# Optimization experiments

Measured on AMD Instinct MI355X. Metric: run time of the kernel, lower is better.

## Reference

```python
import jax, jax.numpy as jnp
import numpy as np
from jax import lax

COND_RATE = 4  # para_cond_downscale_rate
DG = 8        # deformable_groups


def _conv(x, w, b, pad=0, groups=1):
    out = lax.conv_general_dilated(x, w, (1, 1), [(pad, pad), (pad, pad)],
                                   feature_group_count=groups,
                                   dimension_numbers=('NCHW', 'OIHW', 'NCHW'))
    return out + b[None, :, None, None]


def _gn(x, g, b, groups=32, eps=1e-6):
    B, C, H, W = x.shape
    xr = x.reshape(B, groups, C // groups, H * W)
    m = xr.mean(axis=(2, 3), keepdims=True)
    v = ((xr - m) ** 2).mean(axis=(2, 3), keepdims=True)
    xr = (xr - m) * lax.rsqrt(v + eps)
    return xr.reshape(B, C, H, W) * g[None, :, None, None] + b[None, :, None, None]


def _deform_conv2d(x, offset, mask, w, b, dg):
    # x: [B,Cin,H,W], offset: [B,2*dg*9,H,W] (torchvision layout: interleaved y,x per loc),
    # mask: [B,dg*9,H,W], w: [Cout,Cin,3,3]. stride=1, pad=1, dil=1, zero border.
    B, Cin, H, W = x.shape
    K = 9
    Cpg = Cin // dg
    Cout = w.shape[0]
    off = offset.reshape(B, dg, K, 2, H, W)
    ky = (jnp.arange(K) // 3).astype(x.dtype)
    kx = (jnp.arange(K) % 3).astype(x.dtype)
    iy = jnp.arange(H, dtype=x.dtype)
    ix = jnp.arange(W, dtype=x.dtype)
    base_y = iy[None, :, None] - 1.0 + ky[:, None, None]  # [K,H,1]
    base_x = ix[None, None, :] - 1.0 + kx[:, None, None]  # [K,1,W]
    py = off[:, :, :, 0] + base_y[None, None]  # [B,dg,K,H,W]
    px = off[:, :, :, 1] + base_x[None, None]
    y0 = jnp.floor(py)
    x0 = jnp.floor(px)
    ly = py - y0
    lx = px - x0
    xg = x.reshape(B, dg, Cpg, H * W)

    def corner(yc, xc, wt):
        valid = (yc >= 0) & (yc < H) & (xc >= 0) & (xc < W)
        yci = jnp.clip(yc, 0, H - 1).astype(jnp.int32)
        xci = jnp.clip(xc, 0, W - 1).astype(jnp.int32)
        idx = (yci * W + xci).reshape(B, dg, 1, K * H * W)
        v = jnp.take_along_axis(xg, idx, axis=3).reshape(B, dg, Cpg, K, H, W)
        return v * (wt * valid.astype(x.dtype))[:, :, None]

    samp = (corner(y0, x0, (1 - ly) * (1 - lx)) + corner(y0, x0 + 1, (1 - ly) * lx)
            + corner(y0 + 1, x0, ly * (1 - lx)) + corner(y0 + 1, x0 + 1, ly * lx))
    samp = samp * mask.reshape(B, dg, 1, K, H, W)
    wr = w.reshape(Cout, dg, Cpg, K)
    out = jnp.einsum('bgckhw,ogck->bohw', samp, wr)
    return out + b[None, :, None, None]


def setup_inputs() -> dict:
    key = jax.random.key(0)
    ks = jax.random.split(key, 10)
    C = 256
    f32 = jnp.float32
    d = {}
    d['main_feature'] = jax.random.normal(ks[0], (8, C, 64, 64), f32)
    d['condition_feature'] = jax.random.normal(ks[1], (8, C, 16, 16), f32)
    # offset_conv1: 1x1 -> GN -> SiLU -> depthwise 7x7 -> GN -> SiLU -> 1x1
    d['w1'] = jax.random.normal(ks[2], (C, 2 * C, 1, 1), f32) * 0.03
    d['b1'] = jnp.zeros((C,), f32)
    d['g1'] = jnp.ones((C,), f32)
    d['be1'] = jnp.zeros((C,), f32)
    d['w2'] = jax.random.normal(ks[3], (C, 1, 7, 7), f32) * 0.05
    d['b2'] = jnp.zeros((C,), f32)
    d['g2'] = jnp.ones((C,), f32)
    d['be2'] = jnp.zeros((C,), f32)
    d['w3'] = jax.random.normal(ks[4], (C, C, 1, 1), f32) * 0.03
    d['b3'] = jnp.zeros((C,), f32)
    # offset_conv2: 3x3 -> GN -> SiLU
    d['w4'] = jax.random.normal(ks[5], (C, C, 3, 3), f32) * 0.02
    d['b4'] = jnp.zeros((C,), f32)
    d['g3'] = jnp.ones((C,), f32)
    d['be3'] = jnp.zeros((C,), f32)
    # DCNv2Pack conv_offset: 3x3 -> 3*dg*9 = 216 channels (small init -> small offsets)
    d['w_co'] = jax.random.normal(ks[6], (3 * DG * 9, C, 3, 3), f32) * 0.01
    d['b_co'] = jnp.zeros((3 * DG * 9,), f32)
    # DCN main weight
    d['w_dcn'] = jax.random.normal(ks[7], (C, C, 3, 3), f32) * 0.02
    d['b_dcn'] = jnp.zeros((C,), f32)
    return d


def reference(main_feature, condition_feature, w1, b1, g1, be1, w2, b2, g2, be2,
              w3, b3, w4, b4, g3, be3, w_co, b_co, w_dcn, b_dcn):
    B, Cc, h, w_ = condition_feature.shape
    _, Cm, H, W = main_feature.shape
    # note: 2 // cond_downscale_rate == 0 for rate=4, so first resize is identity-sized
    cond = jax.image.resize(condition_feature, (B, Cc, h + 2 // COND_RATE, w_ + 2 // COND_RATE), 'bilinear')
    cond = jax.image.resize(cond, (B, Cc, H, W), 'bilinear')
    f = jnp.concatenate([cond, main_feature], axis=1)
    f = _conv(f, w1, b1)
    f = jax.nn.silu(_gn(f, g1, be1))
    f = _conv(f, w2, b2, pad=3, groups=Cm)  # depthwise 7x7
    f = jax.nn.silu(_gn(f, g2, be2))
    f = _conv(f, w3, b3)
    f = _conv(f, w4, b4, pad=1)
    offset_feat = jax.nn.silu(_gn(f, g3, be3))
    co = _conv(offset_feat, w_co, b_co, pad=1)  # [B, 3*dg*9, H, W]
    o1, o2, m = jnp.split(co, 3, axis=1)
    off = jnp.concatenate([o1, o2], axis=1)     # [B, 2*dg*9, H, W]
    mask = jax.nn.sigmoid(m)
    warp = _deform_conv2d(main_feature, off, mask, w_dcn, b_dcn, DG)
    return (warp, offset_feat)
```

## Files before the change

kernel.cpp:

```cpp
#include <hip/hip_runtime.h>
#include <cstdint>

#define TPB 256

typedef __attribute__((ext_vector_type(8))) short s16x8;
typedef __attribute__((ext_vector_type(4))) short s16x4;
typedef __attribute__((ext_vector_type(4))) float f32x4;

__device__ __forceinline__ float silu_f(float x) { return x / (1.f + __expf(-x)); }

__device__ __forceinline__ short f2bf(float f) {
  union { float f; unsigned u; } v; v.f = f;
  unsigned r = v.u + 0x7fffu + ((v.u >> 16) & 1u);
  return (short)(r >> 16);
}
__device__ __forceinline__ float bf2f(short s) {
  union { unsigned u; float f; } v;
  v.u = ((unsigned)(unsigned short)s) << 16;
  return v.f;
}

__global__ void k_prep_w(const float* __restrict__ w, short* __restrict__ dst,
                         int Cout, int Cin, int taps, int nq, int mode) {
  int idx = blockIdx.x * TPB + threadIdx.x;
  int total = nq * 16 * 64 * 8;
  if (idx >= total) return;
  int j = idx & 7;
  int l = (idx >> 3) & 63;
  int ot = (idx >> 9) & 15;
  int q = idx >> 13;
  int tap, cb;
  if (mode == 0) { int ncb = Cin >> 5; tap = q / ncb; cb = q - tap * ncb; }
  else           { tap = q % 9; cb = q / 9; }
  int o = ot * 16 + (l & 15);
  int c = cb * 32 + ((l >> 4) & 3) * 8 + j;
  float v = 0.f;
  if (o < Cout && c < Cin) v = w[((size_t)o * Cin + c) * taps + tap];
  dst[idx] = f2bf(v);
}

__global__ void k_upsample_nhwc(const float* __restrict__ in, short* __restrict__ outA) {
  int idx = blockIdx.x * TPB + threadIdx.x;
  if (idx >= 8 * 4096 * 256) return;
  int c = idx & 255;
  int p = idx >> 8;
  int b = p >> 12;
  int rem = p & 4095;
  int y = rem >> 6, x = rem & 63;
  float sy = (y + 0.5f) * 0.25f - 0.5f;
  float sx = (x + 0.5f) * 0.25f - 0.5f;
  float y0f = floorf(sy), x0f = floorf(sx);
  float ly = sy - y0f, lx = sx - x0f;
  int y0 = (int)y0f, x0 = (int)x0f;
  int y0c = min(15, max(0, y0)), y1c = min(15, max(0, y0 + 1));
  int x0c = min(15, max(0, x0)), x1c = min(15, max(0, x0 + 1));
  const float* src = in + (size_t)(b * 256 + c) * 256;
  float v00 = src[y0c * 16 + x0c], v01 = src[y0c * 16 + x1c];
  float v10 = src[y1c * 16 + x0c], v11 = src[y1c * 16 + x1c];
  float r = (1.f - ly) * ((1.f - lx) * v00 + lx * v01)
          + ly * ((1.f - lx) * v10 + lx * v11);
  outA[(size_t)p * 512 + c] = f2bf(r);
}

__global__ __launch_bounds__(256) void k_main_tr(const float* __restrict__ in,
    short* __restrict__ xbf, short* __restrict__ outA) {
  const int pc = blockIdx.x, ck = blockIdx.y, b = blockIdx.z;
  __shared__ float sl[32][66];
  const int t = threadIdx.x;
  const int pxl = t & 63, cs = t >> 6;
  const float* src = in + (size_t)(b * 256 + ck * 32) * 4096 + pc * 64;
  #pragma unroll
  for (int i = 0; i < 8; ++i) {
    int c = i * 4 + cs;
    sl[c][pxl] = src[(size_t)c * 4096 + pxl];
  }
  __syncthreads();
  const int oct = (t & 3) * 8, px2 = t >> 2;
  s16x8 v;
  #pragma unroll
  for (int j = 0; j < 8; ++j) v[j] = f2bf(sl[oct + j][px2]);
  size_t p = (size_t)b * 4096 + pc * 64 + px2;
  *(s16x8*)(xbf + p * 256 + ck * 32 + oct) = v;
  *(s16x8*)(outA + p * 512 + 256 + ck * 32 + oct) = v;
}

__global__ __launch_bounds__(256) void k_conv2(
    const short* __restrict__ in, int Cin, int Cout, int taps,
    const short* __restrict__ wf, const float* __restrict__ bias,
    short* __restrict__ out, int remap) {
  const int gid = blockIdx.x;
  const int b = gid & 7;
  const int r = gid >> 3;
  const int og = r & 3, yt = r >> 2;
  const int t = threadIdx.x;
  const int wid = t >> 6, l = t & 63;
  const int wo = wid >> 1, wr = wid & 1;
  const int pd = (taps == 9) ? 1 : 0;
  const int rows_in = 2 + 2 * pd;
  const int pxw = 64 + 2 * pd;
  const int ncb = Cin >> 5;
  const int nchunk = Cin >> 6;
  const int ndy = (taps == 9) ? 3 : 1;
  __shared__ __align__(16) short sl[4 * 66 * 68];
  f32x4 acc[2][4];
  #pragma unroll
  for (int i = 0; i < 2; ++i)
    #pragma unroll
    for (int j = 0; j < 4; ++j) acc[i][j] = (f32x4){0.f, 0.f, 0.f, 0.f};
  const int y0g = yt * 2 - pd;
  for (int chunk = 0; chunk < nchunk; ++chunk) {
    __syncthreads();
    {
      const int nun = rows_in * pxw * 8;
      const int c0 = chunk * 64;
      #pragma unroll
      for (int i = 0; i < 9; ++i) {
        int e = t + i * 256;
        if (e < nun) {
          int oct = e & 7;
          int pe = e >> 3;
          int pxs = pe % pxw;
          int row = pe / pxw;
          int yy = y0g + row, xx = pxs - pd;
          s16x8 v = {0, 0, 0, 0, 0, 0, 0, 0};
          if (yy >= 0 && yy < 64 && xx >= 0 && xx < 64)
            v = *(const s16x8*)(in + (size_t)((b * 64 + yy) * 64 + xx) * Cin
                                + c0 + oct * 8);
          *(s16x8*)(sl + (row * 66 + pxs) * 68 + oct * 8) = v;
        }
      }
    }
    __syncthreads();
    #pragma unroll 2
    for (int cb = 0; cb < 2; ++cb) {
      const int qc = chunk * 2 + cb;
      for (int dyi = 0; dyi < ndy; ++dyi) {
        const int lrow = wr + dyi;
        for (int dxi = 0; dxi < ndy; ++dxi) {
          const int tap = (taps == 9) ? dyi * 3 + dxi : 0;
          const int q = tap * ncb + qc;
          s16x8 afr[2];
          #pragma unroll
          for (int i = 0; i < 2; ++i) {
            int ot = og * 4 + wo * 2 + i;
            afr[i] = *(const s16x8*)(wf + (((size_t)q * 16 + ot) * 64 + l) * 8);
          }
          #pragma unroll
          for (int jt = 0; jt < 4; ++jt) {
            int pxi = jt * 16 + (l & 15) + dxi;
            s16x8 bfr = *(const s16x8*)(sl + (lrow * 66 + pxi) * 68
                                        + cb * 32 + (l >> 4) * 8);
            #pragma unroll
            for (int i = 0; i < 2; ++i)
              acc[i][jt] = __builtin_amdgcn_mfma_f32_16x16x32_bf16(
                  afr[i], bfr, acc[i][jt], 0, 0, 0);
          }
        }
      }
    }
  }
  const int y = yt * 2 + wr;
  #pragma unroll
  for (int i = 0; i < 2; ++i) {
    #pragma unroll
    for (int jt = 0; jt < 4; ++jt) {
      int px = jt * 16 + (l & 15);
      int obase = og * 64 + wo * 32 + i * 16 + (l >> 4) * 4;
      size_t pbase = (size_t)((b * 64 + y) * 64 + px) * (remap ? 256 : Cout);
      if (!remap) {
        s16x4 r2;
        #pragma unroll
        for (int rr = 0; rr < 4; ++rr) r2[rr] = f2bf(acc[i][jt][rr] + bias[obase + rr]);
        *(s16x4*)(out + pbase + obase) = r2;
      } else {
        #pragma unroll
        for (int rr = 0; rr < 4; ++rr) {
          int o = obase + rr;
          if (o < Cout) {
            int op;
            if (o < 144) op = (o / 18) * 32 + (o % 18);
            else { int jj = o - 144; op = (jj / 9) * 32 + 18 + (jj % 9); }
            out[pbase + op] = f2bf(acc[i][jt][rr] + bias[o]);
          }
        }
      }
    }
  }
}

__global__ __launch_bounds__(256) void k_gn_stats(const short* __restrict__ io,
    float* __restrict__ parts) {
  const int gid = blockIdx.x;
  const int b = gid & 7;
  const int r = gid >> 3;
  const int ck = r & 7, g = r >> 3;
  const int t = threadIdx.x;
  float s = 0.f, sq = 0.f;
  #pragma unroll
  for (int i = 0; i < 2; ++i) {
    int e = ck * 512 + t + i * 256;
    s16x8 v = *(const s16x8*)(io + (size_t)(b * 4096 + e) * 256 + g * 8);
    #pragma unroll
    for (int j = 0; j < 8; ++j) { float f = bf2f(v[j]); s += f; sq += f * f; }
  }
  #pragma unroll
  for (int off = 32; off > 0; off >>= 1) {
    s += __shfl_down(s, off);
    sq += __shfl_down(sq, off);
  }
  __shared__ float ps[4], pq[4];
  const int wv = t >> 6, lane = t & 63;
  if (lane == 0) { ps[wv] = s; pq[wv] = sq; }
  __syncthreads();
  if (t == 0) {
    parts[gid * 2]     = ps[0] + ps[1] + ps[2] + ps[3];
    parts[gid * 2 + 1] = pq[0] + pq[1] + pq[2] + pq[3];
  }
}

__global__ __launch_bounds__(256) void k_gn_apply(short* __restrict__ io,
    float* __restrict__ f32out, const float* __restrict__ parts,
    const float* __restrict__ gamma, const float* __restrict__ beta) {
  const int gid = blockIdx.x;
  const int b = gid & 7;
  const int r = gid >> 3;
  const int ck = r & 7, g = r >> 3;
  const int t = threadIdx.x;
  float S = 0.f, Q = 0.f;
  #pragma unroll
  for (int i = 0; i < 8; ++i) {
    int gid2 = (((g << 3) | i) << 3) | b;
    S += parts[gid2 * 2];
    Q += parts[gid2 * 2 + 1];
  }
  const float mean = S * (1.f / 32768.f);
  const float var = Q * (1.f / 32768.f) - mean * mean;
  const float rs = rsqrtf(var + 1e-6f);
  float ga[8], bb[8];
  #pragma unroll
  for (int j = 0; j < 8; ++j) {
    ga[j] = gamma[g * 8 + j] * rs;
    bb[j] = beta[g * 8 + j] - mean * ga[j];
  }
  #pragma unroll
  for (int i = 0; i < 2; ++i) {
    int e = ck * 512 + t + i * 256;
    short* ptr = io + (size_t)(b * 4096 + e) * 256 + g * 8;
    s16x8 v = *(const s16x8*)ptr;
    s16x8 r2;
    #pragma unroll
    for (int j = 0; j < 8; ++j) {
      float o = silu_f(bf2f(v[j]) * ga[j] + bb[j]);
      r2[j] = f2bf(o);
      if (f32out) f32out[(size_t)(b * 256 + g * 8 + j) * 4096 + e] = o;
    }
    *(s16x8*)ptr = r2;
  }
}

__global__ __launch_bounds__(256) void k_dw7_nhwc(const short* __restrict__ in,
    const float* __restrict__ w, const float* __restrict__ bias,
    short* __restrict__ out) {
  const int gid = blockIdx.x;
  const int b = gid & 7;
  const int r = gid >> 3;
  const int ck = r & 7, yt = r >> 3;
  const int t = threadIdx.x;
  const int px = t & 63, oc = t >> 6;
  __shared__ __align__(16) short sl[10 * 70 * 40];
  __shared__ float wl[49 * 32];
  for (int e = t; e < 49 * 32; e += TPB) {
    int tap = e >> 5, cc = e & 31;
    wl[tap * 32 + cc] = w[(ck * 32 + cc) * 49 + tap];
  }
  const int y0in = yt * 4 - 3;
  #pragma unroll
  for (int i = 0; i < 11; ++i) {
    int e = t + i * TPB;
    if (e < 2800) {
      int oc2 = e & 3;
      int pe = e >> 2;
      int pxs = pe % 70;
      int row = pe / 70;
      int yy = y0in + row, xx = pxs - 3;
      s16x8 v = {0, 0, 0, 0, 0, 0, 0, 0};
      if (yy >= 0 && yy < 64 && xx >= 0 && xx < 64)
        v = *(const s16x8*)(in + (size_t)((b * 64 + yy) * 64 + xx) * 256
                            + ck * 32 + oc2 * 8);
      *(s16x8*)(sl + (row * 70 + pxs) * 40 + oc2 * 8) = v;
    }
  }
  __syncthreads();
  float acc[4][8];
  {
    float4 b0 = *(const float4*)(bias + ck * 32 + oc * 8);
    float4 b1 = *(const float4*)(bias + ck * 32 + oc * 8 + 4);
    #pragma unroll
    for (int r2 = 0; r2 < 4; ++r2) {
      acc[r2][0] = b0.x; acc[r2][1] = b0.y; acc[r2][2] = b0.z; acc[r2][3] = b0.w;
      acc[r2][4] = b1.x; acc[r2][5] = b1.y; acc[r2][6] = b1.z; acc[r2][7] = b1.w;
    }
  }
  #pragma unroll
  for (int ky = 0; ky < 7; ++ky) {
    #pragma unroll
    for (int kx = 0; kx < 7; ++kx) {
      const float4 w0 = *(const float4*)(wl + (ky * 7 + kx) * 32 + oc * 8);
      const float4 w1 = *(const float4*)(wl + (ky * 7 + kx) * 32 + oc * 8 + 4);
      #pragma unroll
      for (int r2 = 0; r2 < 4; ++r2) {
        s16x8 v = *(const s16x8*)(sl + ((r2 + ky) * 70 + (px + kx)) * 40 + oc * 8);
        acc[r2][0] += bf2f(v[0]) * w0.x; acc[r2][1] += bf2f(v[1]) * w0.y;
        acc[r2][2] += bf2f(v[2]) * w0.z; acc[r2][3] += bf2f(v[3]) * w0.w;
        acc[r2][4] += bf2f(v[4]) * w1.x; acc[r2][5] += bf2f(v[5]) * w1.y;
        acc[r2][6] += bf2f(v[6]) * w1.z; acc[r2][7] += bf2f(v[7]) * w1.w;
      }
    }
  }
  #pragma unroll
  for (int r2 = 0; r2 < 4; ++r2) {
    int y = yt * 4 + r2;
    s16x8 o;
    #pragma unroll
    for (int j = 0; j < 8; ++j) o[j] = f2bf(acc[r2][j]);
    *(s16x8*)(out + (size_t)((b * 64 + y) * 64 + px) * 256 + ck * 32 + oc * 8) = o;
  }
}

__global__ __launch_bounds__(256) void k_dcn_nhwc(const short* __restrict__ x,
    const short* __restrict__ co, const short* __restrict__ wf,
    const float* __restrict__ bias, float* __restrict__ out) {
  const int gid = blockIdx.x;
  const int b = gid & 7;
  const int r = gid >> 3;
  const int ph = r & 1, y = r >> 1;
  const int t = threadIdx.x;
  const int wid = t >> 6, l = t & 63;
  const int px0 = ph * 32;
  __shared__ __align__(16) short s2[9 * 32 * 40];
  f32x4 acc[4][2];
  #pragma unroll
  for (int i = 0; i < 4; ++i)
    #pragma unroll
    for (int j = 0; j < 2; ++j) acc[i][j] = (f32x4){0.f, 0.f, 0.f, 0.f};
  const short* xb = x + (size_t)b * 4096 * 256;
  for (int g = 0; g < 8; ++g) {
    __syncthreads();
    #pragma unroll
    for (int i = 0; i < 5; ++i) {
      int e = t + i * 256;
      if (e < 1152) {
        int oct = e & 3, pxl = (e >> 2) & 31, k = e >> 7;
        int px = px0 + pxl;
        const short* cp = co + (size_t)(b * 4096 + y * 64 + px) * 256 + g * 32;
        float offy = bf2f(cp[2 * k]);
        float offx = bf2f(cp[2 * k + 1]);
        float mlog = bf2f(cp[18 + k]);
        float mv = 1.f / (1.f + __expf(-mlog));
        float py = offy + (float)(y - 1 + k / 3);
        float pxf = offx + (float)(px - 1 + k % 3);
        float y0f = floorf(py), x0f = floorf(pxf);
        float ly = py - y0f, lx = pxf - x0f;
        int y0 = (int)y0f, x0 = (int)x0f;
        int y1 = y0 + 1, x1 = x0 + 1;
        float fy0 = (y0 >= 0 && y0 < 64) ? 1.f : 0.f;
        float fy1 = (y1 >= 0 && y1 < 64) ? 1.f : 0.f;
        float fx0 = (x0 >= 0 && x0 < 64) ? 1.f : 0.f;
        float fx1 = (x1 >= 0 && x1 < 64) ? 1.f : 0.f;
        float w00 = (1.f - ly) * (1.f - lx) * fy0 * fx0 * mv;
        float w01 = (1.f - ly) * lx * fy0 * fx1 * mv;
        float w10 = ly * (1.f - lx) * fy1 * fx0 * mv;
        float w11 = ly * lx * fy1 * fx1 * mv;
        int y0c = min(63, max(0, y0)), y1c = min(63, max(0, y1));
        int x0c = min(63, max(0, x0)), x1c = min(63, max(0, x1));
        const short* xc = xb + g * 32 + oct * 8;
        s16x8 c00 = *(const s16x8*)(xc + (size_t)(y0c * 64 + x0c) * 256);
        s16x8 c01 = *(const s16x8*)(xc + (size_t)(y0c * 64 + x1c) * 256);
        s16x8 c10 = *(const s16x8*)(xc + (size_t)(y1c * 64 + x0c) * 256);
        s16x8 c11 = *(const s16x8*)(xc + (size_t)(y1c * 64 + x1c) * 256);
        s16x8 pk;
        #pragma unroll
        for (int cc = 0; cc < 8; ++cc) {
          float v = w00 * bf2f(c00[cc]) + w01 * bf2f(c01[cc])
                  + w10 * bf2f(c10[cc]) + w11 * bf2f(c11[cc]);
          pk[cc] = f2bf(v);
        }
        *(s16x8*)(s2 + (k * 32 + pxl) * 40 + oct * 8) = pk;
      }
    }
    __syncthreads();
    #pragma unroll
    for (int k = 0; k < 9; ++k) {
      const int q = g * 9 + k;
      s16x8 afr[4], bfr[2];
      #pragma unroll
      for (int i = 0; i < 4; ++i)
        afr[i] = *(const s16x8*)(wf + (((size_t)q * 16 + wid * 4 + i) * 64 + l) * 8);
      #pragma unroll
      for (int jt = 0; jt < 2; ++jt)
        bfr[jt] = *(const s16x8*)(s2 + (k * 32 + jt * 16 + (l & 15)) * 40 + (l >> 4) * 8);
      #pragma unroll
      for (int i = 0; i < 4; ++i)
        #pragma unroll
        for (int jt = 0; jt < 2; ++jt)
          acc[i][jt] = __builtin_amdgcn_mfma_f32_16x16x32_bf16(
              afr[i], bfr[jt], acc[i][jt], 0, 0, 0);
    }
  }
  #pragma unroll
  for (int i = 0; i < 4; ++i) {
    int obase = wid * 64 + i * 16 + (l >> 4) * 4;
    #pragma unroll
    for (int jt = 0; jt < 2; ++jt) {
      int pxo = px0 + jt * 16 + (l & 15);
      #pragma unroll
      for (int rr = 0; rr < 4; ++rr) {
        int o = obase + rr;
        out[(((size_t)b * 256 + o) * 64 + y) * 64 + pxo] = acc[i][jt][rr] + bias[o];
      }
    }
  }
}

extern "C" void kernel_launch(void* const* d_in, const int* in_sizes, int n_in,
                              void* d_out, int out_size, void* d_ws, size_t ws_size,
                              hipStream_t stream) {
  const float* main_f = (const float*)d_in[0];
  const float* cond   = (const float*)d_in[1];
  const float* w1  = (const float*)d_in[2];
  const float* b1  = (const float*)d_in[3];
  const float* g1  = (const float*)d_in[4];
  const float* be1 = (const float*)d_in[5];
  const float* w2  = (const float*)d_in[6];
  const float* b2  = (const float*)d_in[7];
  const float* g2  = (const float*)d_in[8];
  const float* be2 = (const float*)d_in[9];
  const float* w3  = (const float*)d_in[10];
  const float* b3  = (const float*)d_in[11];
  const float* w4  = (const float*)d_in[12];
  const float* b4  = (const float*)d_in[13];
  const float* g3  = (const float*)d_in[14];
  const float* be3 = (const float*)d_in[15];
  const float* w_co  = (const float*)d_in[16];
  const float* b_co  = (const float*)d_in[17];
  const float* w_dcn = (const float*)d_in[18];
  const float* b_dcn = (const float*)d_in[19];

  float* out = (float*)d_out;
  float* warp_out = out;
  float* offset_feat = out + 8388608;

  short* ws = (short*)d_ws;
  short* bufA  = ws;
  short* Bb    = bufA + 16777216;
  short* xbf   = Bb + 8388608;
  short* wf1   = xbf + 8388608;
  short* wf3   = wf1 + 131072;
  short* wf4   = wf3 + 65536;
  short* wfco  = wf4 + 589824;
  short* wfdcn = wfco + 589824;
  float* gparts = (float*)(wfdcn + 589824);

  auto cdiv = [](int a, int b) { return (a + b - 1) / b; };

  k_prep_w<<<cdiv(16 * 8192, TPB), TPB, 0, stream>>>(w1, wf1, 256, 512, 1, 16, 0);
  k_prep_w<<<cdiv(8 * 8192, TPB), TPB, 0, stream>>>(w3, wf3, 256, 256, 1, 8, 0);
  k_prep_w<<<cdiv(72 * 8192, TPB), TPB, 0, stream>>>(w4, wf4, 256, 256, 9, 72, 0);
  k_prep_w<<<cdiv(72 * 8192, TPB), TPB, 0, stream>>>(w_co, wfco, 216, 256, 9, 72, 0);
  k_prep_w<<<cdiv(72 * 8192, TPB), TPB, 0, stream>>>(w_dcn, wfdcn, 256, 256, 9, 72, 1);

  k_upsample_nhwc<<<cdiv(8 * 4096 * 256, TPB), TPB, 0, stream>>>(cond, bufA);
  dim3 gtr(64, 8, 8);
  k_main_tr<<<gtr, TPB, 0, stream>>>(main_f, xbf, bufA);

  k_conv2<<<1024, TPB, 0, stream>>>(bufA, 512, 256, 1, wf1, b1, Bb, 0);
  k_gn_stats<<<2048, TPB, 0, stream>>>(Bb, gparts);
  k_gn_apply<<<2048, TPB, 0, stream>>>(Bb, nullptr, gparts, g1, be1);
  k_dw7_nhwc<<<1024, TPB, 0, stream>>>(Bb, w2, b2, bufA);
  k_gn_stats<<<2048, TPB, 0, stream>>>(bufA, gparts);
  k_gn_apply<<<2048, TPB, 0, stream>>>(bufA, nullptr, gparts, g2, be2);
  k_conv2<<<1024, TPB, 0, stream>>>(bufA, 256, 256, 1, wf3, b3, Bb, 0);
  k_conv2<<<1024, TPB, 0, stream>>>(Bb, 256, 256, 9, wf4, b4, bufA, 0);
  k_gn_stats<<<2048, TPB, 0, stream>>>(bufA, gparts);
  k_gn_apply<<<2048, TPB, 0, stream>>>(bufA, offset_feat, gparts, g3, be3);
  k_conv2<<<1024, TPB, 0, stream>>>(bufA, 256, 216, 9, wfco, b_co, Bb, 1);
  k_dcn_nhwc<<<1024, TPB, 0, stream>>>(xbf, Bb, wfdcn, b_dcn, warp_out);
}
```

Before: 456.3 us.

## Precompute DCN bilinear weights once per sample and merge weight-prep launches

The deformable conv sampling stage previously recomputed offsets, sigmoid mask, bilinear weights and clamped indices in each of the four channel-octet threads. Those values are now computed once per (tap, pixel) into shared memory, behind an extra barrier, and the octet threads read them back. Separately, the five weight-repacking kernels are fused into a single launch that dispatches on the flat index. This cuts redundant ALU work and launch overhead at the cost of about 10KB more LDS per block and one more __syncthreads per group.

```diff
diff --git a/kernel.cpp b/kernel.cpp
--- a/kernel.cpp
+++ b/kernel.cpp
@@ -20,15 +20,21 @@
   return v.f;
 }
 
-__global__ void k_prep_w(const float* __restrict__ w, short* __restrict__ dst,
-                         int Cout, int Cin, int taps, int nq, int mode) {
+__global__ void k_prep_all(const float* __restrict__ w1, const float* __restrict__ w3,
+                           const float* __restrict__ w4, const float* __restrict__ wco,
+                           const float* __restrict__ wdcn, short* __restrict__ dst) {
   int idx = blockIdx.x * TPB + threadIdx.x;
-  int total = nq * 16 * 64 * 8;
-  if (idx >= total) return;
-  int j = idx & 7;
-  int l = (idx >> 3) & 63;
-  int ot = (idx >> 9) & 15;
-  int q = idx >> 13;
+  if (idx >= 1966080) return;
+  const float* w; int Cout, Cin, taps, mode; int local = idx;
+  if (idx < 131072)       { w = w1;   Cout = 256; Cin = 512; taps = 1; mode = 0; }
+  else if (idx < 196608)  { w = w3;   local -= 131072;  Cout = 256; Cin = 256; taps = 1; mode = 0; }
+  else if (idx < 786432)  { w = w4;   local -= 196608;  Cout = 256; Cin = 256; taps = 9; mode = 0; }
+  else if (idx < 1376256) { w = wco;  local -= 786432;  Cout = 216; Cin = 256; taps = 9; mode = 0; }
+  else                    { w = wdcn; local -= 1376256; Cout = 256; Cin = 256; taps = 9; mode = 1; }
+  int j = local & 7;
+  int l = (local >> 3) & 63;
+  int ot = (local >> 9) & 15;
+  int q = local >> 13;
   int tap, cb;
   if (mode == 0) { int ncb = Cin >> 5; tap = q / ncb; cb = q - tap * ncb; }
   else           { tap = q % 9; cb = q / 9; }
@@ -338,6 +344,7 @@
   const int wid = t >> 6, l = t & 63;
   const int px0 = ph * 32;
   __shared__ __align__(16) short s2[9 * 32 * 40];
+  __shared__ unsigned swt[288 * 9];
   f32x4 acc[4][2];
   #pragma unroll
   for (int i = 0; i < 4; ++i)
@@ -347,10 +354,10 @@
   for (int g = 0; g < 8; ++g) {
     __syncthreads();
     #pragma unroll
-    for (int i = 0; i < 5; ++i) {
-      int e = t + i * 256;
-      if (e < 1152) {
-        int oct = e & 3, pxl = (e >> 2) & 31, k = e >> 7;
+    for (int i = 0; i < 2; ++i) {
+      int e2 = t + i * 256;
+      if (e2 < 288) {
+        int pxl = e2 & 31, k = e2 >> 5;
         int px = px0 + pxl;
         const short* cp = co + (size_t)(b * 4096 + y * 64 + px) * 256 + g * 32;
         float offy = bf2f(cp[2 * k]);
@@ -373,11 +380,33 @@
         float w11 = ly * lx * fy1 * fx1 * mv;
         int y0c = min(63, max(0, y0)), y1c = min(63, max(0, y1));
         int x0c = min(63, max(0, x0)), x1c = min(63, max(0, x1));
+        unsigned* wp = swt + e2 * 9;
+        wp[0] = __float_as_uint(w00);
+        wp[1] = __float_as_uint(w01);
+        wp[2] = __float_as_uint(w10);
+        wp[3] = __float_as_uint(w11);
+        wp[4] = (unsigned)((y0c * 64 + x0c) * 256);
+        wp[5] = (unsigned)((y0c * 64 + x1c) * 256);
+        wp[6] = (unsigned)((y1c * 64 + x0c) * 256);
+        wp[7] = (unsigned)((y1c * 64 + x1c) * 256);
+      }
+    }
+    __syncthreads();
+    #pragma unroll
+    for (int i = 0; i < 5; ++i) {
+      int e = t + i * 256;
+      if (e < 1152) {
+        int oct = e & 3, pxl = (e >> 2) & 31, k = e >> 7;
+        const unsigned* wp = swt + (k * 32 + pxl) * 9;
+        float w00 = __uint_as_float(wp[0]);
+        float w01 = __uint_as_float(wp[1]);
+        float w10 = __uint_as_float(wp[2]);
+        float w11 = __uint_as_float(wp[3]);
         const short* xc = xb + g * 32 + oct * 8;
-        s16x8 c00 = *(const s16x8*)(xc + (size_t)(y0c * 64 + x0c) * 256);
-        s16x8 c01 = *(const s16x8*)(xc + (size_t)(y0c * 64 + x1c) * 256);
-        s16x8 c10 = *(const s16x8*)(xc + (size_t)(y1c * 64 + x0c) * 256);
-        s16x8 c11 = *(const s16x8*)(xc + (size_t)(y1c * 64 + x1c) * 256);
+        s16x8 c00 = *(const s16x8*)(xc + wp[4]);
+        s16x8 c01 = *(const s16x8*)(xc + wp[5]);
+        s16x8 c10 = *(const s16x8*)(xc + wp[6]);
+        s16x8 c11 = *(const s16x8*)(xc + wp[7]);
         s16x8 pk;
         #pragma unroll
         for (int cc = 0; cc < 8; ++cc) {
@@ -454,7 +483,8 @@
   short* bufA  = ws;
   short* Bb    = bufA + 16777216;
   short* xbf   = Bb + 8388608;
-  short* wf1   = xbf + 8388608;
+  short* wfall = xbf + 8388608;
+  short* wf1   = wfall;
   short* wf3   = wf1 + 131072;
   short* wf4   = wf3 + 65536;
   short* wfco  = wf4 + 589824;
@@ -463,11 +493,7 @@
 
   auto cdiv = [](int a, int b) { return (a + b - 1) / b; };
 
-  k_prep_w<<<cdiv(16 * 8192, TPB), TPB, 0, stream>>>(w1, wf1, 256, 512, 1, 16, 0);
-  k_prep_w<<<cdiv(8 * 8192, TPB), TPB, 0, stream>>>(w3, wf3, 256, 256, 1, 8, 0);
-  k_prep_w<<<cdiv(72 * 8192, TPB), TPB, 0, stream>>>(w4, wf4, 256, 256, 9, 72, 0);
-  k_prep_w<<<cdiv(72 * 8192, TPB), TPB, 0, stream>>>(w_co, wfco, 216, 256, 9, 72, 0);
-  k_prep_w<<<cdiv(72 * 8192, TPB), TPB, 0, stream>>>(w_dcn, wfdcn, 256, 256, 9, 72, 1);
+  k_prep_all<<<cdiv(1966080, TPB), TPB, 0, stream>>>(w1, w3, w4, w_co, w_dcn, wfall);
 
   k_upsample_nhwc<<<cdiv(8 * 4096 * 256, TPB), TPB, 0, stream>>>(cond, bufA);
   dim3 gtr(64, 8, 8);
```

Result: faster. 446.3 us (median of 2 runs) (-2.2%).
